# Performance work log

Hardware: AMD Instinct MI355X
Metric: run time of the kernel (lower is better)

The kernel has to match this reference:

```python
import jax, jax.numpy as jnp
import numpy as np
from jax import lax

CHANNELS = 64
STRIDE = (2, 2, 2)
PAD = ((1, 1), (1, 1), (1, 1))  # zero pad, filt_size=3 -> pad 1 each side per spatial dim


def make_blur_filter(channels: int) -> jnp.ndarray:
    # binomial filter for filt_size=3: [1,2,1]; 3D separable outer product, normalized
    a = np.array([1.0, 2.0, 1.0], dtype=np.float32)
    f = a[:, None, None] * a[None, :, None] * a[None, None, :]
    f = f / f.sum()
    # depthwise conv kernel, OIDHW with O=channels, I=1
    return jnp.asarray(np.broadcast_to(f[None, None], (channels, 1, 3, 3, 3)).copy())


def setup_inputs() -> dict:
    key = jax.random.key(0)
    x = jax.random.normal(key, (2, CHANNELS, 64, 96, 96), dtype=jnp.float32)
    filt = make_blur_filter(CHANNELS)
    return {"x": x, "filt": filt}


def reference(x, filt):
    # zero-pad + depthwise (grouped) 3D conv with stride 2, matching
    # F.conv3d(pad(inp), filt, stride=2, groups=C)
    return lax.conv_general_dilated(
        x, filt,
        window_strides=STRIDE,
        padding=PAD,
        dimension_numbers=("NCDHW", "OIDHW", "NCDHW"),
        feature_group_count=x.shape[1],
    )
```

## Files before the change

kernel.cpp:

```cpp
#include <hip/hip_runtime.h>


namespace {
constexpr int D = 64, H = 96, W = 96;
constexpr int OD = 32, OH = 48, OW = 48;
constexpr int HW = H * W;
constexpr int PLANE_THREADS = OH * OW;
}

__global__ __launch_bounds__(256) void blurpool3d_kernel(
    const float* __restrict__ in, float* __restrict__ out)
{
    const int p = blockIdx.x * 256 + threadIdx.x;
    const int x = p % OW;
    const int y = p / OW;
    const long nc = blockIdx.y;

    const float* __restrict__ inp = in + nc * (long)(D * HW);
    float* __restrict__ outp = out + nc * (long)(OD * OH * OW);

    const int xb = 2 * x - 1;
    const int yb = 2 * y - 1;
    const bool has_left = (x > 0);

    float a = 0.0f;

    for (int z = 0; z < OD; ++z) {
        const float* p0 = inp + (2 * z) * HW;
        const float* p1 = p0 + HW;
        float b = 0.0f, c = 0.0f;
        #pragma unroll
        for (int dy = 0; dy < 3; ++dy) {
            const int yy = yb + dy;
            if (yy >= 0) {
                const float wy = (dy == 1) ? 2.0f : 1.0f;
                const float* r0 = p0 + yy * W + xb;
                const float* r1 = p1 + yy * W + xb;
                const float l0 = has_left ? r0[0] : 0.0f;
                const float l1 = has_left ? r1[0] : 0.0f;
                b += wy * (l0 + 2.0f * r0[1] + r0[2]);
                c += wy * (l1 + 2.0f * r1[1] + r1[2]);
            }
        }
        outp[((long)z * OH + y) * OW + x] = (a + 2.0f * b + c) * (1.0f / 64.0f);
        a = c;
    }
}

extern "C" void kernel_launch(void* const* d_in, const int* in_sizes, int n_in,
                              void* d_out, int out_size, void* d_ws, size_t ws_size,
                              hipStream_t stream)
{
    const float* x = (const float*)d_in[0];
    float* out = (float*)d_out;
    dim3 grid(PLANE_THREADS / 256, 128);
    blurpool3d_kernel<<<grid, dim3(256), 0, stream>>>(x, out);
}
```

Measured before the change: 432.5 us.

## Vectorize blurpool to 4 outputs per thread and split depth into chunks

Each thread now computes four adjacent output columns using float4 loads of eight input values plus one left halo, and stores its outputs as float4. The depth loop is split into chunks of 8 output planes across a new grid dimension, with the leading plane recomputed at each chunk boundary. This cuts load instruction count and exposes more blocks than the old 9x128 grid, which ran the full depth serially per thread. The price is some redundant plane reads at chunk edges and a changed 12x16 block shape.

```diff
diff --git a/kernel.cpp b/kernel.cpp
--- a/kernel.cpp
+++ b/kernel.cpp
@@ -5,44 +5,61 @@
 constexpr int D = 64, H = 96, W = 96;
 constexpr int OD = 32, OH = 48, OW = 48;
 constexpr int HW = H * W;
-constexpr int PLANE_THREADS = OH * OW;
+constexpr int YB = 16;
+constexpr int ZCH = 8;
 }
 
-__global__ __launch_bounds__(256) void blurpool3d_kernel(
+typedef float f4 __attribute__((ext_vector_type(4)));
+
+__global__ __launch_bounds__(192) void blurpool3d_kernel(
     const float* __restrict__ in, float* __restrict__ out)
 {
-    const int p = blockIdx.x * 256 + threadIdx.x;
-    const int x = p % OW;
-    const int y = p / OW;
-    const long nc = blockIdx.y;
+    const int xg = threadIdx.x;
+    const int yl = threadIdx.y;
+    const int y  = blockIdx.x * YB + yl;
+    const int z0 = blockIdx.y * ZCH;
+    const long nc = blockIdx.z;
 
     const float* __restrict__ inp = in + nc * (long)(D * HW);
-    float* __restrict__ outp = out + nc * (long)(OD * OH * OW);
+    float* __restrict__ outp = out + nc * (long)(OD * OH * OW)
+                                   + (long)y * OW + xg * 4;
 
-    const int xb = 2 * x - 1;
+    const int xb = xg * 8;
     const int yb = 2 * y - 1;
-    const bool has_left = (x > 0);
+    const int r0i = (y > 0) ? yb : 0;
+    const float w0 = (y > 0) ? 1.0f : 0.0f;
+    const int r1i = yb + 1, r2i = yb + 2;
+    const bool has_left = (xg > 0);
 
-    float a = 0.0f;
+    auto rowconv = [&](const float* plane, int row) -> f4 {
+        const float* r = plane + row * W + xb;
+        f4 A = *(const f4*)(r);
+        f4 B = *(const f4*)(r + 4);
+        float h0 = has_left ? r[-1] : 0.0f;
+        f4 b;
+        b.x = h0  + 2.0f * A.x + A.y;
+        b.y = A.y + 2.0f * A.z + A.w;
+        b.z = A.w + 2.0f * B.x + B.y;
+        b.w = B.y + 2.0f * B.z + B.w;
+        return b;
+    };
 
-    for (int z = 0; z < OD; ++z) {
-        const float* p0 = inp + (2 * z) * HW;
-        const float* p1 = p0 + HW;
-        float b = 0.0f, c = 0.0f;
-        #pragma unroll
-        for (int dy = 0; dy < 3; ++dy) {
-            const int yy = yb + dy;
-            if (yy >= 0) {
-                const float wy = (dy == 1) ? 2.0f : 1.0f;
-                const float* r0 = p0 + yy * W + xb;
-                const float* r1 = p1 + yy * W + xb;
-                const float l0 = has_left ? r0[0] : 0.0f;
-                const float l1 = has_left ? r1[0] : 0.0f;
-                b += wy * (l0 + 2.0f * r0[1] + r0[2]);
-                c += wy * (l1 + 2.0f * r1[1] + r1[2]);
-            }
-        }
-        outp[((long)z * OH + y) * OW + x] = (a + 2.0f * b + c) * (1.0f / 64.0f);
+    auto planeconv = [&](const float* plane) -> f4 {
+        f4 ra = rowconv(plane, r0i);
+        f4 rb = rowconv(plane, r1i);
+        f4 rc = rowconv(plane, r2i);
+        return w0 * ra + 2.0f * rb + rc;
+    };
+
+    f4 a = {0.0f, 0.0f, 0.0f, 0.0f};
+    if (z0 != 0) a = planeconv(inp + (2 * z0 - 1) * HW);
+
+    for (int zi = 0; zi < ZCH; ++zi) {
+        const int z = z0 + zi;
+        f4 b = planeconv(inp + (2 * z) * HW);
+        f4 c = planeconv(inp + (2 * z + 1) * HW);
+        f4 o = (a + 2.0f * b + c) * 0.015625f;
+        *(f4*)(outp + (long)z * (OH * OW)) = o;
         a = c;
     }
 }
@@ -53,6 +70,7 @@
 {
     const float* x = (const float*)d_in[0];
     float* out = (float*)d_out;
-    dim3 grid(PLANE_THREADS / 256, 128);
-    blurpool3d_kernel<<<grid, dim3(256), 0, stream>>>(x, out);
+    dim3 grid(OH / YB, OD / ZCH, 128);
+    dim3 block(12, YB);
+    blurpool3d_kernel<<<grid, block, 0, stream>>>(x, out);
 }
```

Result: faster. 410.9 us (-5.0%).
